# Performance work log

Measured on AMD Instinct MI355X. Metric: run time of the kernel, lower is better.

Reference implementation:

```python
import jax, jax.numpy as jnp
import numpy as np

B, S, D, H = 2, 2048, 2048, 16
HD = D // H  # 128


def apply_rotary(xq, xk, cos, sin):
    # xq, xk: [B, S, H, HD]; cos, sin: [S, HD//2]
    def rot(x):
        xr = x.astype(jnp.float32).reshape(*x.shape[:-1], -1, 2)  # [B,S,H,HD/2,2]
        xe, xo = xr[..., 0], xr[..., 1]
        c = cos[None, :, None, :]
        s = sin[None, :, None, :]
        out_e = xe * c - xo * s
        out_o = xe * s + xo * c
        out = jnp.stack([out_e, out_o], axis=-1).reshape(x.shape)
        return out.astype(x.dtype)
    return rot(xq), rot(xk)


def setup_inputs() -> dict:
    key = jax.random.key(0)
    ks = jax.random.split(key, 8)
    x = jax.random.normal(ks[0], (B, S, D), dtype=jnp.float32)
    scale = 1.0 / np.sqrt(D)
    wq = jax.random.normal(ks[1], (D, D), dtype=jnp.float32) * scale
    wk = jax.random.normal(ks[2], (D, D), dtype=jnp.float32) * scale
    wv = jax.random.normal(ks[3], (D, D), dtype=jnp.float32) * scale
    wo = jax.random.normal(ks[4], (D, D), dtype=jnp.float32) * scale
    # RoPE frequencies (standard LLaMA): theta = 10000
    inv_freq = 1.0 / (10000.0 ** (np.arange(0, HD, 2, dtype=np.float32) / HD))
    t = np.arange(S, dtype=np.float32)
    ang = np.outer(t, inv_freq)  # [S, HD/2]
    freqs_cos = jnp.asarray(np.cos(ang))
    freqs_sin = jnp.asarray(np.sin(ang))
    # causal additive mask [1,1,S,S]
    neg = jnp.full((S, S), -1e9, dtype=jnp.float32)
    mask = jnp.triu(neg, k=1)[None, None, :, :]
    return {"x": x, "start_pos": 0, "freqs_cos": freqs_cos, "freqs_sin": freqs_sin,
            "mask": mask, "wq": wq, "wk": wk, "wv": wv, "wo": wo}


def reference(x, start_pos, freqs_cos, freqs_sin, mask, wq, wk, wv, wo):
    bsz, seqlen, dim = x.shape
    xq = (x @ wq.T).reshape(bsz, seqlen, H, HD)
    xk = (x @ wk.T).reshape(bsz, seqlen, H, HD)
    xv = (x @ wv.T).reshape(bsz, seqlen, H, HD)
    xq, xk = apply_rotary(xq, xk, freqs_cos, freqs_sin)
    # [B,H,S,HD]
    q = xq.transpose(0, 2, 1, 3)
    k = xk.transpose(0, 2, 1, 3)
    v = xv.transpose(0, 2, 1, 3)
    scores = jnp.einsum('bhqd,bhkd->bhqk', q, k) / jnp.sqrt(jnp.float32(HD))
    scores = scores + mask
    probs = jax.nn.softmax(scores.astype(jnp.float32), axis=-1).astype(q.dtype)
    out = jnp.einsum('bhqk,bhkd->bhqd', probs, v)
    out = out.transpose(0, 2, 1, 3).reshape(bsz, seqlen, dim)
    return out @ wo.T
```

## Files before the change

kernel.cpp:

```cpp
#include <hip/hip_runtime.h>
#include <cstdint>

typedef unsigned short u16;
typedef __attribute__((ext_vector_type(8))) short bf16x8;
typedef __attribute__((ext_vector_type(4))) float f32x4;

#define S_LEN 2048
#define DM    2048
#define NH    16
#define HDIM  128

__device__ __forceinline__ u16 f2bf(float f) {
  union { float f; unsigned u; } v; v.f = f;
  unsigned r = v.u + 0x7fffu + ((v.u >> 16) & 1u);
  return (u16)(r >> 16);
}
__device__ __forceinline__ float bf2f(u16 h) {
  union { unsigned u; float f; } v; v.u = ((unsigned)h) << 16;
  return v.f;
}

typedef __attribute__((address_space(3))) void lds_void_t;
typedef const __attribute__((address_space(1))) void gbl_void_t;
__device__ __forceinline__ void gload_lds16(const void* g, void* l) {
  __builtin_amdgcn_global_load_lds((gbl_void_t*)g, (lds_void_t*)l, 16, 0, 0);
}

#define VMCNTN(nn) asm volatile("s_waitcnt vmcnt(%0)" :: "n"(nn) : "memory")

__global__ void cvt5_k(const float* s0, u16* d0, int n0,
                       const float* s1, u16* d1, int n1,
                       const float* s2, u16* d2, int n2,
                       const float* s3, u16* d3, int n3,
                       const float* s4, u16* d4, int n4) {
  const int stride = gridDim.x * blockDim.x;
  const int tid = blockIdx.x * blockDim.x + threadIdx.x;
#define CVT(S, D, N)                                        \
  for (int i = tid; i < ((N) >> 2); i += stride) {          \
    float4 v = ((const float4*)(S))[i];                     \
    ushort4 o;                                              \
    o.x = f2bf(v.x); o.y = f2bf(v.y);                       \
    o.z = f2bf(v.z); o.w = f2bf(v.w);                       \
    ((ushort4*)(D))[i] = o;                                 \
  }
  CVT(s0, d0, n0) CVT(s1, d1, n1) CVT(s2, d2, n2)
  CVT(s3, d3, n3) CVT(s4, d4, n4)
#undef CVT
}

template <int BM, int BN, int M, int N, int K, typename CT>
__global__ __launch_bounds__(512, 2) void gemm8(const u16* __restrict__ A,
                                                const u16* __restrict__ Bm,
                                                CT* __restrict__ C) {
  constexpr int PWM = BM / 2, PWN = BN / 4;
  constexpr int MR = PWM / 16, NR = PWN / 16, NB = NR / 2;
  constexpr int LA = BM / 128, LB = BN / 128;
  constexpr int VM = LA + LB;
  constexpr int nbn = N / BN, nbm = M / BM;
  constexpr int nwg = nbm * nbn;
  constexpr int GM = 8;
  __shared__ u16 sA[4 * BM * 32];
  __shared__ u16 sB[4 * BN * 32];

  const int t = threadIdx.x;
  const int lane = t & 63, wid = t >> 6;
  const int r0 = lane & 15, kq = lane >> 4;
  const int wr = wid >> 2, wc = wid & 3;

  const int bid = blockIdx.x;
  const int wgl = (bid & 7) * (nwg >> 3) + (bid >> 3);
  const int gid = wgl / (GM * nbn);
  const int rem = wgl % (GM * nbn);
  const long tile_m = (long)(gid * GM + (rem & (GM - 1))) * BM;
  const long tile_n = (long)(rem >> 3) * BN;

  constexpr int NT = K >> 6;
  constexpr int NITER = NT >> 1;

  const int swzcol = ((t & 3) ^ ((t >> 3) & 3)) * 8;
  const u16* gA = A + (tile_m + (t >> 2)) * (long)K + swzcol;
  const u16* gB = Bm + (tile_n + (t >> 2)) * (long)K + swzcol;

  auto stageA = [&](int kt, int kh) {
    u16* base = &sA[((kt & 1) * 2 + kh) * (BM * 32)] + wid * 512;
#pragma unroll
    for (int r = 0; r < LA; ++r)
      gload_lds16(gA + (long)(r * 128) * K + kt * 64 + kh * 32, base + r * 4096);
  };
  auto stageB = [&](int kt, int kh) {
    u16* base = &sB[((kt & 1) * 2 + kh) * (BN * 32)] + wid * 512;
#pragma unroll
    for (int r = 0; r < LB; ++r)
      gload_lds16(gB + (long)(r * 128) * K + kt * 64 + kh * 32, base + r * 4096);
  };

  const int rdslot = (kq ^ ((r0 >> 1) & 3)) * 8;
  const int aoff = (wr * PWM + r0) * 32 + rdslot;
  const int boff = (wc * PWN + r0) * 32 + rdslot;

  f32x4 acc[MR][NR];
#pragma unroll
  for (int m = 0; m < MR; ++m)
#pragma unroll
    for (int n = 0; n < NR; ++n) acc[m][n] = (f32x4){0.f, 0.f, 0.f, 0.f};

  stageA(0, 0); stageB(0, 0); stageA(0, 1); stageB(0, 1);
  stageA(1, 0); stageB(1, 0);
  VMCNTN(VM);
  __builtin_amdgcn_s_barrier();

#define PH(KT, KH, G, STAGE_STMT, VM_STMT)                                  \
  {                                                                         \
    const u16* ra = &sA[(((KT) & 1) * 2 + (KH)) * (BM * 32)] + aoff;        \
    const u16* rb = &sB[(((KT) & 1) * 2 + (KH)) * (BN * 32)] + boff;        \
    if ((G) == 0) {                                                         \
      _Pragma("unroll") for (int m = 0; m < MR; ++m)                        \
          a[m] = *(const bf16x8*)(ra + m * 512);                            \
    }                                                                       \
    _Pragma("unroll") for (int n = 0; n < NB; ++n)                          \
        b[n] = *(const bf16x8*)(rb + ((G) * NB + n) * 512);                 \
    STAGE_STMT;                                                             \
    VM_STMT;                                                                \
    __builtin_amdgcn_s_barrier();                                           \
    __builtin_amdgcn_s_setprio(1);                                          \
    _Pragma("unroll") for (int m = 0; m < MR; ++m)                          \
        _Pragma("unroll") for (int n = 0; n < NB; ++n)                      \
            acc[m][(G) * NB + n] = __builtin_amdgcn_mfma_f32_16x16x32_bf16( \
                a[m], b[n], acc[m][(G) * NB + n], 0, 0, 0);                 \
    __builtin_amdgcn_s_setprio(0);                                          \
    __builtin_amdgcn_s_barrier();                                           \
  }

  for (int it = 0; it < NITER; ++it) {
    const int kt0 = 2 * it, kt1 = 2 * it + 1;
    const bool last = (it == NITER - 1);
    bf16x8 a[MR], b[NB];
    PH(kt0, 0, 0, stageA(kt1, 1), ((void)0));
    PH(kt0, 0, 1, stageB(kt1, 1), ((void)0));
    PH(kt0, 1, 0, { if (kt0 + 2 < NT) stageA(kt0 + 2, 0); }, ((void)0));
    PH(kt0, 1, 1, { if (kt0 + 2 < NT) stageB(kt0 + 2, 0); },
       { if (last) { VMCNTN(0); } else { VMCNTN(VM); } });
    PH(kt1, 0, 0, { if (kt0 + 2 < NT) stageA(kt0 + 2, 1); }, ((void)0));
    PH(kt1, 0, 1, { if (kt0 + 2 < NT) stageB(kt0 + 2, 1); }, ((void)0));
    PH(kt1, 1, 0, { if (kt0 + 3 < NT) stageA(kt0 + 3, 0); }, ((void)0));
    PH(kt1, 1, 1, { if (kt0 + 3 < NT) stageB(kt0 + 3, 0); }, VMCNTN(VM));
  }
#undef PH

#pragma unroll
  for (int m = 0; m < MR; ++m)
#pragma unroll
    for (int n = 0; n < NR; ++n)
#pragma unroll
      for (int r = 0; r < 4; ++r) {
        long grow = tile_m + wr * PWM + m * 16 + kq * 4 + r;
        long gcol = tile_n + wc * PWN + n * 16 + r0;
        float v = acc[m][n][r];
        if constexpr (sizeof(CT) == 2) C[grow * N + gcol] = (CT)f2bf(v);
        else                           C[grow * N + gcol] = v;
      }
}

__global__ void rope_k(const u16* __restrict__ qkv, const float* __restrict__ cosT,
                       const float* __restrict__ sinT, u16* __restrict__ qt,
                       u16* __restrict__ kt) {
  int z = blockIdx.y;
  long idx = (long)blockIdx.x * blockDim.x + threadIdx.x;
  int hd2 = (int)(idx & 63);
  int s   = (int)((idx >> 6) & (S_LEN - 1));
  int bh  = (int)(idx >> 17);
  int b = bh >> 4, h = bh & 15;
  const u16* src = qkv + ((long)(b * S_LEN + s)) * 6144 + z * 2048 + h * HDIM + hd2 * 2;
  ushort2 p = *(const ushort2*)src;
  float e = bf2f(p.x), o = bf2f(p.y);
  float c = cosT[s * 64 + hd2], sn = sinT[s * 64 + hd2];
  float oe = e * c - o * sn;
  float oo = e * sn + o * c;
  if (z == 0) {
    const float sc = 0.12751743202f;
    oe *= sc; oo *= sc;
  }
  u16* dst = (z ? kt : qt) + ((long)bh * S_LEN + s) * HDIM + hd2 * 2;
  ushort2 w; w.x = f2bf(oe); w.y = f2bf(oo);
  *(ushort2*)dst = w;
}

__global__ void vtrans_k(const u16* __restrict__ qkv, u16* __restrict__ vt) {
  __shared__ u16 tile[64][65];
  int bh = blockIdx.z;
  int b = bh >> 4, h = bh & 15;
  int s0 = blockIdx.x * 64, d0 = blockIdx.y * 64;
  int tx = threadIdx.x, ty = threadIdx.y;
#pragma unroll
  for (int i = 0; i < 64; i += 4) {
    int s = s0 + ty + i;
    tile[ty + i][tx] = qkv[((long)(b * S_LEN + s)) * 6144 + 4096 + h * HDIM + d0 + tx];
  }
  __syncthreads();
#pragma unroll
  for (int i = 0; i < 64; i += 4) {
    int d = d0 + ty + i;
    vt[((long)bh * HDIM + d) * S_LEN + s0 + tx] = tile[tx][ty + i];
  }
}

__global__ __launch_bounds__(128) void flash_k(const u16* __restrict__ qt,
                                               const u16* __restrict__ kt,
                                               const u16* __restrict__ vt,
                                               u16* __restrict__ attn) {
  constexpr int PS = 40;
  __shared__ u16 pbuf[2][2][32 * PS];
  const int t = threadIdx.x, lane = t & 63, wid = t >> 6;
  const int r0 = lane & 15, kq = lane >> 4;
  const int bh = blockIdx.x, b = bh >> 4, h = bh & 15;
  const int tile = (gridDim.y - 1) - blockIdx.y;
  const int q0w = tile * 64 + wid * 32;
  const int crow = kq * 4;

  const u16* qb = qt + ((long)bh * S_LEN + q0w) * HDIM;
  const u16* kb = kt + (long)bh * S_LEN * HDIM;
  const u16* vb = vt + (long)bh * HDIM * S_LEN;
  u16* pb0 = &pbuf[0][wid][0];
  u16* pb1 = &pbuf[1][wid][0];

  bf16x8 aq[2][4];
#pragma unroll
  for (int qc = 0; qc < 2; ++qc)
#pragma unroll
    for (int kk = 0; kk < 4; ++kk)
      aq[qc][kk] = *(const bf16x8*)(qb + (qc * 16 + r0) * HDIM + kk * 32 + kq * 8);

  f32x4 o[2][8];
  float mrow[2] = {-1e30f, -1e30f}, lrow[2] = {0.f, 0.f};
#pragma unroll
  for (int qc = 0; qc < 2; ++qc)
#pragma unroll
    for (int dt = 0; dt < 8; ++dt) o[qc][dt] = (f32x4){0.f, 0.f, 0.f, 0.f};

  bf16x8 bkA[2][4], bkB[2][4], bvA[8], bvB[8];
  f32x4 saccA[2][2], saccB[2][2];

  auto loadK = [&](bf16x8 (&dst)[2][4], int kv) {
#pragma unroll
    for (int kc = 0; kc < 2; ++kc)
#pragma unroll
      for (int kk = 0; kk < 4; ++kk)
        dst[kc][kk] = *(const bf16x8*)(kb + (long)(kv + kc * 16 + r0) * HDIM + kk * 32 + kq * 8);
  };
  auto loadV = [&](bf16x8 (&dst)[8], int kv) {
#pragma unroll
    for (int dt = 0; dt < 8; ++dt)
      dst[dt] = *(const bf16x8*)(vb + (long)(dt * 16 + r0) * S_LEN + kv + kq * 8);
  };
  auto qk = [&](bf16x8 (&kf)[2][4], f32x4 (&sacc)[2][2]) {
    __builtin_amdgcn_s_setprio(1);
#pragma unroll
    for (int kc = 0; kc < 2; ++kc) {
      f32x4 a0 = (f32x4){0.f, 0.f, 0.f, 0.f};
      f32x4 a1 = (f32x4){0.f, 0.f, 0.f, 0.f};
#pragma unroll
      for (int kk = 0; kk < 4; ++kk) {
        a0 = __builtin_amdgcn_mfma_f32_16x16x32_bf16(kf[kc][kk], aq[0][kk], a0, 0, 0, 0);
        a1 = __builtin_amdgcn_mfma_f32_16x16x32_bf16(kf[kc][kk], aq[1][kk], a1, 0, 0, 0);
      }
      sacc[kc][0] = a0; sacc[kc][1] = a1;
    }
    __builtin_amdgcn_s_setprio(0);
  };
  auto softmax_store = [&](f32x4 (&sacc)[2][2], int kv0, u16* pb) {
    const bool diag = (kv0 == q0w);
#pragma unroll
    for (int qc = 0; qc < 2; ++qc) {
      float s[2][4];
#pragma unroll
      for (int kc = 0; kc < 2; ++kc)
#pragma unroll
        for (int r = 0; r < 4; ++r) {
          float v = sacc[kc][qc][r];
          if (diag && (kc * 16 + crow + r > qc * 16 + r0)) v = -1e30f;
          s[kc][r] = v;
        }
      float pm = fmaxf(fmaxf(fmaxf(s[0][0], s[0][1]), fmaxf(s[0][2], s[0][3])),
                       fmaxf(fmaxf(s[1][0], s[1][1]), fmaxf(s[1][2], s[1][3])));
      pm = fmaxf(pm, __shfl_xor(pm, 16));
      pm = fmaxf(pm, __shfl_xor(pm, 32));
      if (!__all(pm - mrow[qc] <= 11.5416f)) {
        float mnew = fmaxf(mrow[qc], pm);
        float co = exp2f(mrow[qc] - mnew);
        mrow[qc] = mnew;
        lrow[qc] *= co;
        float cod[4];
#pragma unroll
        for (int r = 0; r < 4; ++r)
          cod[r] = __shfl(co, (lane & 48) | (crow + r));
#pragma unroll
        for (int dt = 0; dt < 8; ++dt)
#pragma unroll
          for (int r = 0; r < 4; ++r)
            o[qc][dt][r] *= cod[r];
      }
      float p[2][4];
      float rs = 0.f;
#pragma unroll
      for (int kc = 0; kc < 2; ++kc)
#pragma unroll
        for (int r = 0; r < 4; ++r) {
          p[kc][r] = exp2f(s[kc][r] - mrow[qc]);
          rs += p[kc][r];
        }
      rs += __shfl_xor(rs, 16);
      rs += __shfl_xor(rs, 32);
      lrow[qc] += rs;
#pragma unroll
      for (int kc = 0; kc < 2; ++kc) {
        unsigned w0, w1;
        asm("v_cvt_pk_bf16_f32 %0, %1, %2" : "=v"(w0) : "v"(p[kc][0]), "v"(p[kc][1]));
        asm("v_cvt_pk_bf16_f32 %0, %1, %2" : "=v"(w1) : "v"(p[kc][2]), "v"(p[kc][3]));
        uint2 w; w.x = w0; w.y = w1;
        *(uint2*)(pb + (qc * 16 + r0) * PS + kc * 16 + crow) = w;
      }
    }
  };
  auto pv = [&](const u16* pb, bf16x8 (&bv)[8]) {
    bf16x8 pa0 = *(const bf16x8*)(pb + r0 * PS + kq * 8);
    bf16x8 pa1 = *(const bf16x8*)(pb + (16 + r0) * PS + kq * 8);
    __builtin_amdgcn_s_setprio(1);
#pragma unroll
    for (int dt = 0; dt < 8; ++dt) {
      o[0][dt] = __builtin_amdgcn_mfma_f32_16x16x32_bf16(pa0, bv[dt], o[0][dt], 0, 0, 0);
      o[1][dt] = __builtin_amdgcn_mfma_f32_16x16x32_bf16(pa1, bv[dt], o[1][dt], 0, 0, 0);
    }
    __builtin_amdgcn_s_setprio(0);
  };

  loadK(bkA, 0);
  if (32 <= q0w) loadK(bkB, 32);
  qk(bkA, saccA);
  int kv0 = 0;
  for (;;) {
    {
      const bool more = (kv0 + 32 <= q0w);
      loadV(bvA, kv0);
      softmax_store(saccA, kv0, pb0);
      if (more) qk(bkB, saccB);
      if (kv0 + 64 <= q0w) loadK(bkA, kv0 + 64);
      pv(pb0, bvA);
      kv0 += 32;
      if (!more) break;
    }
    {
      const bool more = (kv0 + 32 <= q0w);
      loadV(bvB, kv0);
      softmax_store(saccB, kv0, pb1);
      if (more) qk(bkA, saccA);
      if (kv0 + 64 <= q0w) loadK(bkB, kv0 + 64);
      pv(pb1, bvB);
      kv0 += 32;
      if (!more) break;
    }
  }

#pragma unroll
  for (int qc = 0; qc < 2; ++qc) {
    float linv[4];
#pragma unroll
    for (int r = 0; r < 4; ++r)
      linv[r] = 1.0f / __shfl(lrow[qc], (lane & 48) | (crow + r));
#pragma unroll
    for (int dt = 0; dt < 8; ++dt)
#pragma unroll
      for (int r = 0; r < 4; ++r) {
        int srow = q0w + qc * 16 + crow + r;
        attn[((long)(b * S_LEN + srow)) * DM + h * HDIM + dt * 16 + r0] =
            f2bf(o[qc][dt][r] * linv[r]);
      }
  }
}

extern "C" void kernel_launch(void* const* d_in, const int* in_sizes, int n_in,
                              void* d_out, int out_size, void* d_ws, size_t ws_size,
                              hipStream_t stream) {
  (void)in_sizes; (void)n_in; (void)out_size; (void)ws_size;
  const float* x  = (const float*)d_in[0];
  const float* fc = (const float*)d_in[2];
  const float* fs = (const float*)d_in[3];
  const float* wq = (const float*)d_in[5];
  const float* wk = (const float*)d_in[6];
  const float* wv = (const float*)d_in[7];
  const float* wo = (const float*)d_in[8];
  float* out = (float*)d_out;

  u16* xb   = (u16*)d_ws;
  u16* wqkv = xb + 8388608;
  u16* wob  = wqkv + 12582912;
  u16* qkv  = wob + 4194304;
  u16* qt   = qkv + 25165824;
  u16* kt   = qt + 8388608;
  u16* vt   = kt + 8388608;
  u16* attn = qkv;

  cvt5_k<<<2048, 256, 0, stream>>>(x, xb, 8388608,
                                   wq, wqkv, 4194304,
                                   wk, wqkv + 4194304, 4194304,
                                   wv, wqkv + 8388608, 4194304,
                                   wo, wob, 4194304);

  gemm8<256, 256, 4096, 6144, 2048, u16><<<384, 512, 0, stream>>>(xb, wqkv, qkv);

  rope_k<<<dim3(16384, 2), 256, 0, stream>>>(qkv, fc, fs, qt, kt);
  vtrans_k<<<dim3(32, 2, 32), dim3(64, 4), 0, stream>>>(qkv, vt);

  flash_k<<<dim3(32, 32), 128, 0, stream>>>(qt, kt, vt, attn);

  gemm8<128, 256, 4096, 2048, 2048, float><<<256, 512, 0, stream>>>(attn, wob, out);
}
```

Before: 330.5 us.

## Shrink flash attention blocks to one wave covering sixteen query rows

Each flash attention workgroup goes from two waves with 32 query rows each to a single wave with 16 query rows, and the grid grows fourfold. The aim is more independent waves in flight and finer causal load balancing, with less idle tail time per CU. The cost is that each K and V fragment loaded from memory now feeds half as many MFMAs, doubling K/V load traffic per unit of compute. The causal mask test is generalised because a 32-wide KV step can now straddle the diagonal.

Result: slower. 444.3 us (+34.4%).

```diff
diff --git a/kernel.cpp b/kernel.cpp
--- a/kernel.cpp
+++ b/kernel.cpp
@@ -204,41 +204,37 @@
   }
 }
 
-__global__ __launch_bounds__(128) void flash_k(const u16* __restrict__ qt,
-                                               const u16* __restrict__ kt,
-                                               const u16* __restrict__ vt,
-                                               u16* __restrict__ attn) {
+__global__ __launch_bounds__(64) void flash_k(const u16* __restrict__ qt,
+                                              const u16* __restrict__ kt,
+                                              const u16* __restrict__ vt,
+                                              u16* __restrict__ attn) {
   constexpr int PS = 40;
-  __shared__ u16 pbuf[2][2][32 * PS];
-  const int t = threadIdx.x, lane = t & 63, wid = t >> 6;
+  __shared__ u16 pbuf[2][16 * PS];
+  const int lane = threadIdx.x & 63;
   const int r0 = lane & 15, kq = lane >> 4;
   const int bh = blockIdx.x, b = bh >> 4, h = bh & 15;
-  const int tile = (gridDim.y - 1) - blockIdx.y;
-  const int q0w = tile * 64 + wid * 32;
+  const int seg = (gridDim.y - 1) - blockIdx.y;
+  const int q0w = seg * 16;
   const int crow = kq * 4;
 
   const u16* qb = qt + ((long)bh * S_LEN + q0w) * HDIM;
   const u16* kb = kt + (long)bh * S_LEN * HDIM;
   const u16* vb = vt + (long)bh * HDIM * S_LEN;
-  u16* pb0 = &pbuf[0][wid][0];
-  u16* pb1 = &pbuf[1][wid][0];
-
-  bf16x8 aq[2][4];
-#pragma unroll
-  for (int qc = 0; qc < 2; ++qc)
-#pragma unroll
-    for (int kk = 0; kk < 4; ++kk)
-      aq[qc][kk] = *(const bf16x8*)(qb + (qc * 16 + r0) * HDIM + kk * 32 + kq * 8);
-
-  f32x4 o[2][8];
-  float mrow[2] = {-1e30f, -1e30f}, lrow[2] = {0.f, 0.f};
-#pragma unroll
-  for (int qc = 0; qc < 2; ++qc)
-#pragma unroll
-    for (int dt = 0; dt < 8; ++dt) o[qc][dt] = (f32x4){0.f, 0.f, 0.f, 0.f};
+  u16* pb0 = &pbuf[0][0];
+  u16* pb1 = &pbuf[1][0];
+
+  bf16x8 aq[4];
+#pragma unroll
+  for (int kk = 0; kk < 4; ++kk)
+    aq[kk] = *(const bf16x8*)(qb + r0 * HDIM + kk * 32 + kq * 8);
+
+  f32x4 o[8];
+  float mrow = -1e30f, lrow = 0.f;
+#pragma unroll
+  for (int dt = 0; dt < 8; ++dt) o[dt] = (f32x4){0.f, 0.f, 0.f, 0.f};
 
   bf16x8 bkA[2][4], bkB[2][4], bvA[8], bvB[8];
-  f32x4 saccA[2][2], saccB[2][2];
+  f32x4 saccA[2], saccB[2];
 
   auto loadK = [&](bf16x8 (&dst)[2][4], int kv) {
 #pragma unroll
@@ -252,84 +248,75 @@
     for (int dt = 0; dt < 8; ++dt)
       dst[dt] = *(const bf16x8*)(vb + (long)(dt * 16 + r0) * S_LEN + kv + kq * 8);
   };
-  auto qk = [&](bf16x8 (&kf)[2][4], f32x4 (&sacc)[2][2]) {
+  auto qk = [&](bf16x8 (&kf)[2][4], f32x4 (&sacc)[2]) {
     __builtin_amdgcn_s_setprio(1);
 #pragma unroll
     for (int kc = 0; kc < 2; ++kc) {
       f32x4 a0 = (f32x4){0.f, 0.f, 0.f, 0.f};
-      f32x4 a1 = (f32x4){0.f, 0.f, 0.f, 0.f};
-#pragma unroll
-      for (int kk = 0; kk < 4; ++kk) {
-        a0 = __builtin_amdgcn_mfma_f32_16x16x32_bf16(kf[kc][kk], aq[0][kk], a0, 0, 0, 0);
-        a1 = __builtin_amdgcn_mfma_f32_16x16x32_bf16(kf[kc][kk], aq[1][kk], a1, 0, 0, 0);
+#pragma unroll
+      for (int kk = 0; kk < 4; ++kk)
+        a0 = __builtin_amdgcn_mfma_f32_16x16x32_bf16(kf[kc][kk], aq[kk], a0, 0, 0, 0);
+      sacc[kc] = a0;
+    }
+    __builtin_amdgcn_s_setprio(0);
+  };
+  auto softmax_store = [&](f32x4 (&sacc)[2], int kv0, u16* pb) {
+    const bool needm = (kv0 + 31 > q0w);
+    float s[2][4];
+#pragma unroll
+    for (int kc = 0; kc < 2; ++kc)
+#pragma unroll
+      for (int r = 0; r < 4; ++r) {
+        float v = sacc[kc][r];
+        if (needm && (kv0 + kc * 16 + crow + r > q0w + r0)) v = -1e30f;
+        s[kc][r] = v;
       }
-      sacc[kc][0] = a0; sacc[kc][1] = a1;
-    }
-    __builtin_amdgcn_s_setprio(0);
-  };
-  auto softmax_store = [&](f32x4 (&sacc)[2][2], int kv0, u16* pb) {
-    const bool diag = (kv0 == q0w);
-#pragma unroll
-    for (int qc = 0; qc < 2; ++qc) {
-      float s[2][4];
-#pragma unroll
-      for (int kc = 0; kc < 2; ++kc)
-#pragma unroll
-        for (int r = 0; r < 4; ++r) {
-          float v = sacc[kc][qc][r];
-          if (diag && (kc * 16 + crow + r > qc * 16 + r0)) v = -1e30f;
-          s[kc][r] = v;
-        }
-      float pm = fmaxf(fmaxf(fmaxf(s[0][0], s[0][1]), fmaxf(s[0][2], s[0][3])),
-                       fmaxf(fmaxf(s[1][0], s[1][1]), fmaxf(s[1][2], s[1][3])));
-      pm = fmaxf(pm, __shfl_xor(pm, 16));
-      pm = fmaxf(pm, __shfl_xor(pm, 32));
-      if (!__all(pm - mrow[qc] <= 11.5416f)) {
-        float mnew = fmaxf(mrow[qc], pm);
-        float co = exp2f(mrow[qc] - mnew);
-        mrow[qc] = mnew;
-        lrow[qc] *= co;
-        float cod[4];
+    float pm = fmaxf(fmaxf(fmaxf(s[0][0], s[0][1]), fmaxf(s[0][2], s[0][3])),
+                     fmaxf(fmaxf(s[1][0], s[1][1]), fmaxf(s[1][2], s[1][3])));
+    pm = fmaxf(pm, __shfl_xor(pm, 16));
+    pm = fmaxf(pm, __shfl_xor(pm, 32));
+    if (!__all(pm - mrow <= 11.5416f)) {
+      float mnew = fmaxf(mrow, pm);
+      float co = exp2f(mrow - mnew);
+      mrow = mnew;
+      lrow *= co;
+      float cod[4];
+#pragma unroll
+      for (int r = 0; r < 4; ++r)
+        cod[r] = __shfl(co, (lane & 48) | (crow + r));
+#pragma unroll
+      for (int dt = 0; dt < 8; ++dt)
 #pragma unroll
         for (int r = 0; r < 4; ++r)
-          cod[r] = __shfl(co, (lane & 48) | (crow + r));
-#pragma unroll
-        for (int dt = 0; dt < 8; ++dt)
-#pragma unroll
-          for (int r = 0; r < 4; ++r)
-            o[qc][dt][r] *= cod[r];
+          o[dt][r] *= cod[r];
+    }
+    float p[2][4];
+    float rs = 0.f;
+#pragma unroll
+    for (int kc = 0; kc < 2; ++kc)
+#pragma unroll
+      for (int r = 0; r < 4; ++r) {
+        p[kc][r] = exp2f(s[kc][r] - mrow);
+        rs += p[kc][r];
       }
-      float p[2][4];
-      float rs = 0.f;
-#pragma unroll
-      for (int kc = 0; kc < 2; ++kc)
-#pragma unroll
-        for (int r = 0; r < 4; ++r) {
-          p[kc][r] = exp2f(s[kc][r] - mrow[qc]);
-          rs += p[kc][r];
-        }
-      rs += __shfl_xor(rs, 16);
-      rs += __shfl_xor(rs, 32);
-      lrow[qc] += rs;
-#pragma unroll
-      for (int kc = 0; kc < 2; ++kc) {
-        unsigned w0, w1;
-        asm("v_cvt_pk_bf16_f32 %0, %1, %2" : "=v"(w0) : "v"(p[kc][0]), "v"(p[kc][1]));
-        asm("v_cvt_pk_bf16_f32 %0, %1, %2" : "=v"(w1) : "v"(p[kc][2]), "v"(p[kc][3]));
-        uint2 w; w.x = w0; w.y = w1;
-        *(uint2*)(pb + (qc * 16 + r0) * PS + kc * 16 + crow) = w;
-      }
+    rs += __shfl_xor(rs, 16);
+    rs += __shfl_xor(rs, 32);
+    lrow += rs;
+#pragma unroll
+    for (int kc = 0; kc < 2; ++kc) {
+      unsigned w0, w1;
+      asm("v_cvt_pk_bf16_f32 %0, %1, %2" : "=v"(w0) : "v"(p[kc][0]), "v"(p[kc][1]));
+      asm("v_cvt_pk_bf16_f32 %0, %1, %2" : "=v"(w1) : "v"(p[kc][2]), "v"(p[kc][3]));
+      uint2 w; w.x = w0; w.y = w1;
+      *(uint2*)(pb + r0 * PS + kc * 16 + crow) = w;
     }
   };
   auto pv = [&](const u16* pb, bf16x8 (&bv)[8]) {
     bf16x8 pa0 = *(const bf16x8*)(pb + r0 * PS + kq * 8);
-    bf16x8 pa1 = *(const bf16x8*)(pb + (16 + r0) * PS + kq * 8);
     __builtin_amdgcn_s_setprio(1);
 #pragma unroll
-    for (int dt = 0; dt < 8; ++dt) {
-      o[0][dt] = __builtin_amdgcn_mfma_f32_16x16x32_bf16(pa0, bv[dt], o[0][dt], 0, 0, 0);
-      o[1][dt] = __builtin_amdgcn_mfma_f32_16x16x32_bf16(pa1, bv[dt], o[1][dt], 0, 0, 0);
-    }
+    for (int dt = 0; dt < 8; ++dt)
+      o[dt] = __builtin_amdgcn_mfma_f32_16x16x32_bf16(pa0, bv[dt], o[dt], 0, 0, 0);
     __builtin_amdgcn_s_setprio(0);
   };
 
@@ -360,21 +347,18 @@
     }
   }
 
-#pragma unroll
-  for (int qc = 0; qc < 2; ++qc) {
-    float linv[4];
-#pragma unroll
-    for (int r = 0; r < 4; ++r)
-      linv[r] = 1.0f / __shfl(lrow[qc], (lane & 48) | (crow + r));
-#pragma unroll
-    for (int dt = 0; dt < 8; ++dt)
-#pragma unroll
-      for (int r = 0; r < 4; ++r) {
-        int srow = q0w + qc * 16 + crow + r;
-        attn[((long)(b * S_LEN + srow)) * DM + h * HDIM + dt * 16 + r0] =
-            f2bf(o[qc][dt][r] * linv[r]);
-      }
-  }
+  float linv[4];
+#pragma unroll
+  for (int r = 0; r < 4; ++r)
+    linv[r] = 1.0f / __shfl(lrow, (lane & 48) | (crow + r));
+#pragma unroll
+  for (int dt = 0; dt < 8; ++dt)
+#pragma unroll
+    for (int r = 0; r < 4; ++r) {
+      int srow = q0w + crow + r;
+      attn[((long)(b * S_LEN + srow)) * DM + h * HDIM + dt * 16 + r0] =
+          f2bf(o[dt][r] * linv[r]);
+    }
 }
 
 extern "C" void kernel_launch(void* const* d_in, const int* in_sizes, int n_in,
@@ -410,7 +394,7 @@
   rope_k<<<dim3(16384, 2), 256, 0, stream>>>(qkv, fc, fs, qt, kt);
   vtrans_k<<<dim3(32, 2, 32), dim3(64, 4), 0, stream>>>(qkv, vt);
 
-  flash_k<<<dim3(32, 32), 128, 0, stream>>>(qt, kt, vt, attn);
+  flash_k<<<dim3(32, 128), 64, 0, stream>>>(qt, kt, vt, attn);
 
   gemm8<128, 256, 4096, 2048, 2048, float><<<256, 512, 0, stream>>>(attn, wob, out);
 }
```
